# Optimization experiments

Measured on AMD Instinct MI355X. Metric: run time of the kernel, lower is better.

Reference implementation:

```python
import jax, jax.numpy as jnp
import numpy as np

V, D, K, NB, T = 50257, 128, 3, 8, 64
DIV_W = 2.0  # diversity_weight


def setup_inputs() -> dict:
    key = jax.random.key(0)
    k1, k2, k3 = jax.random.split(key, 3)
    tokens = jax.random.randint(k1, (T,), 0, V)
    E = jax.random.normal(k2, (V, D), jnp.float32)          # embedding table
    bubbles = 1.5 * jax.random.normal(k3, (K, NB, D), jnp.float32)  # init_spread_foam scale=1.5
    decay_base = jnp.asarray(0.8, jnp.float32)
    sensitivity = jnp.asarray(1.0, jnp.float32)
    return {"tokens": tokens, "E": E, "bubbles": bubbles,
            "decay_base": decay_base, "sensitivity": sensitivity}


def reference(tokens, E, bubbles, decay_base, sensitivity):
    d = E.shape[1]
    inv_sqrt_d = 1.0 / jnp.sqrt(jnp.asarray(d, jnp.float32))
    # normalized bubble states (pure-state directions), fixed over time
    psi = bubbles / (jnp.linalg.norm(bubbles, axis=-1, keepdims=True) + 1e-10)  # [K,NB,D]

    def step(memories, tok):
        # memories: [K, NB, D]
        x = E[tok]  # [D]
        mem_mean = memories.mean(axis=1)  # [K, D]
        mem_norm = jnp.linalg.norm(mem_mean, axis=-1) + 1e-10  # [K]
        x_norm = jnp.linalg.norm(x) + 1e-10
        cos = (mem_mean @ x) / (x_norm * mem_norm)  # [K]
        novelty = jnp.where(mem_norm > 1e-8, 1.0 - cos, 1.0)  # [K]
        decay = jax.nn.sigmoid(decay_base - jnp.abs(sensitivity) * novelty)  # [K]
        xm = x[None, :] + decay[:, None] * mem_mean  # [K, D]

        # foam forward (vectorized over K foams)
        scores = DIV_W * jnp.einsum('knd,kd->kn', bubbles, xm) * inv_sqrt_d  # [K,NB]
        w = jax.nn.softmax(scores, axis=-1)  # [K,NB]
        rho_k = jnp.einsum('kn,knd,kne->kde', w, psi, psi)  # [K,D,D] PSD, trace 1
        eq = w[..., None] * xm[:, None, :] + (1.0 - w)[..., None] * bubbles  # [K,NB,D]
        new_mem = decay[:, None, None] * memories + (1.0 - decay)[:, None, None] * eq

        rho = rho_k.mean(axis=0)  # [D,D] ensemble mixture
        eigs = jnp.clip(jnp.linalg.eigvalsh(rho), 1e-12)
        eigs = eigs / eigs.sum()
        logits = jnp.einsum('vd,de,ve->v', E, rho, E)  # born rule, [V]
        token_probs = jax.nn.softmax(logits)
        S_rho = -(eigs * jnp.clip(jnp.log(eigs), -100.0)).sum()
        H_tokens = -(token_probs * jnp.clip(jnp.log(token_probs), -100.0)).sum()
        F_tokens = H_tokens - S_rho
        logits_k = jnp.einsum('vd,kde,ve->kv', E, rho_k, E)  # [K,V]
        per_foam_probs = jax.nn.softmax(logits_k, axis=-1)
        return new_mem, (token_probs, rho, S_rho, H_tokens, F_tokens, per_foam_probs)

    mem0 = jnp.zeros((bubbles.shape[0], bubbles.shape[1], E.shape[1]), E.dtype)
    _, outs = jax.lax.scan(step, mem0, tokens)
    # outs: token_probs [T,V], rho [T,D,D], S_rho [T], H_tokens [T], F_tokens [T], per_foam_probs [T,K,V]
    return outs
```

## Files before the change

### kernel.cpp

```cpp
#include <hip/hip_runtime.h>
#include <math.h>

namespace {
constexpr int Vv  = 50257;
constexpr int Dc  = 128;
constexpr int Kc  = 3;
constexpr int NBc = 8;
constexpr int Jc  = 24;
constexpr int Tc  = 64;
constexpr int CHV = 1024;
constexpr int NCH = (Vv + CHV - 1) / CHV;
constexpr float INV_SQRT_D = 0.08838834764831845f;
constexpr float DIVW = 2.0f;

constexpr size_t WS_PSI  = 0;
constexpr size_t WS_G    = 4096;
constexpr size_t WS_BB   = 5120;
constexpr size_t WS_XN   = 6144;
constexpr size_t WS_BX   = 6400;
constexpr size_t WS_WALL = 8192;
constexpr size_t WS_PART = 12288;
constexpr size_t WS_LOGZ = 45056;
constexpr size_t WS_P2T  = 65536;

constexpr size_t OFF_TOK = 0;
constexpr size_t OFF_RHO = (size_t)Tc * Vv;
constexpr size_t OFF_S   = OFF_RHO + (size_t)Tc * Dc * Dc;
constexpr size_t OFF_H   = OFF_S + Tc;
constexpr size_t OFF_F   = OFF_H + Tc;
constexpr size_t OFF_PF  = OFF_F + Tc;
}

__device__ __forceinline__ float wsum64(float v) {
#pragma unroll
  for (int m = 1; m < 64; m <<= 1) v += __shfl_xor(v, m);
  return v;
}

__device__ __forceinline__ void comb(float& m1, float& s1, float m2, float s2) {
  float M = fmaxf(m1, m2);
  float e1 = (s1 > 0.f) ? expf(m1 - M) : 0.f;
  float e2 = (s2 > 0.f) ? expf(m2 - M) : 0.f;
  s1 = s1 * e1 + s2 * e2;
  m1 = M;
}
__device__ __forceinline__ void comb_sl(float& m1, float& s1, float& sl1,
                                        float m2, float s2, float sl2) {
  float M = fmaxf(m1, m2);
  float e1 = (s1 > 0.f) ? expf(m1 - M) : 0.f;
  float e2 = (s2 > 0.f) ? expf(m2 - M) : 0.f;
  s1 = s1 * e1 + s2 * e2;
  sl1 = sl1 * e1 + sl2 * e2;
  m1 = M;
}

__global__ void k_prep(const float* __restrict__ bub, float* __restrict__ ws) {
  __shared__ float braw[Jc * Dc];
  __shared__ float psi[Jc * Dc];
  __shared__ float nrm[Jc];
  int tid = threadIdx.x;
  for (int i = tid; i < Jc * Dc; i += 256) braw[i] = bub[i];
  __syncthreads();
  if (tid < Jc) {
    float s = 0.f;
    for (int d = 0; d < Dc; ++d) { float b = braw[tid * Dc + d]; s += b * b; }
    nrm[tid] = sqrtf(s) + 1e-10f;
  }
  __syncthreads();
  for (int i = tid; i < Jc * Dc; i += 256) {
    float v = braw[i] / nrm[i / Dc];
    psi[i] = v;
    ws[WS_PSI + i] = v;
  }
  __syncthreads();
  for (int i = tid; i < Jc * Jc; i += 256) {
    int r = i / Jc, c = i % Jc;
    float g = 0.f, b = 0.f;
    for (int d = 0; d < Dc; ++d) {
      g += psi[r * Dc + d] * psi[c * Dc + d];
      b += braw[r * Dc + d] * braw[c * Dc + d];
    }
    ws[WS_G + i] = g;
    ws[WS_BB + i] = b;
  }
}

__global__ void k_tok(const int* __restrict__ tok, const float* __restrict__ E,
                      const float* __restrict__ bub, float* __restrict__ ws) {
  int t = blockIdx.x, lane = threadIdx.x;
  int tk = tok[t];
  float eA = E[(size_t)tk * Dc + lane];
  float eB = E[(size_t)tk * Dc + 64 + lane];
  float xn = wsum64(eA * eA + eB * eB);
  if (lane == 0) ws[WS_XN + t] = xn;
  float p[Jc];
#pragma unroll
  for (int j = 0; j < Jc; ++j)
    p[j] = bub[j * Dc + lane] * eA + bub[j * Dc + 64 + lane] * eB;
#pragma unroll
  for (int j = 0; j < Jc; ++j) p[j] = wsum64(p[j]);
  if (lane == 0) {
#pragma unroll
    for (int j = 0; j < Jc; ++j) ws[WS_BX + (size_t)t * Jc + j] = p[j];
  }
}

__global__ void k_recur(const int* __restrict__ tok, const float* __restrict__ E,
                        const float* __restrict__ bub, const float* __restrict__ pdb,
                        const float* __restrict__ psn, float* __restrict__ ws) {
  __shared__ float sBX[Tc * Jc];
  __shared__ float sXN[Tc];
  int lane = threadIdx.x;
  for (int i = lane; i < Tc * Jc; i += 64) sBX[i] = ws[WS_BX + i];
  if (lane < Tc) sXN[lane] = ws[WS_XN + lane];
  float db = pdb[0];
  float sens = fabsf(psn[0]);
  int tokv = tok[lane];
  float bubA[Jc], bubB[Jc];
#pragma unroll
  for (int j = 0; j < Jc; ++j) {
    bubA[j] = bub[j * Dc + lane];
    bubB[j] = bub[j * Dc + 64 + lane];
  }
  int jme = (lane < Jc) ? lane : (Jc - 1);
  int kme = jme >> 3;
  float BBrow[Jc];
#pragma unroll
  for (int j = 0; j < Jc; ++j) BBrow[j] = ws[WS_BB + (size_t)jme * Jc + j];
  __syncthreads();
  float mmA[Kc] = {0.f, 0.f, 0.f}, mmB[Kc] = {0.f, 0.f, 0.f};
  float BMv[Kc] = {0.f, 0.f, 0.f};
  int tk0 = __shfl(tokv, 0);
  float xA = E[(size_t)tk0 * Dc + lane];
  float xB = E[(size_t)tk0 * Dc + 64 + lane];
  for (int t = 0; t < Tc; ++t) {
    float nxA = 0.f, nxB = 0.f;
    if (t + 1 < Tc) {
      int nk = __shfl(tokv, t + 1);
      nxA = E[(size_t)nk * Dc + lane];
      nxB = E[(size_t)nk * Dc + 64 + lane];
    }
    float dk[Kc], nk2[Kc];
#pragma unroll
    for (int k = 0; k < Kc; ++k) {
      dk[k]  = wsum64(mmA[k] * xA + mmB[k] * xB);
      nk2[k] = wsum64(mmA[k] * mmA[k] + mmB[k] * mmB[k]);
    }
    float xn = sqrtf(sXN[t]) + 1e-10f;
    float dec[Kc], xmA[Kc], xmB[Kc];
#pragma unroll
    for (int k = 0; k < Kc; ++k) {
      float mn = sqrtf(nk2[k]) + 1e-10f;
      float cosv = dk[k] / (xn * mn);
      float nov = (mn > 1e-8f) ? (1.f - cosv) : 1.f;
      dec[k] = 1.f / (1.f + expf(-(db - sens * nov)));
      xmA[k] = xA + dec[k] * mmA[k];
      xmB[k] = xB + dec[k] * mmB[k];
    }
    float bxj = sBX[t * Jc + jme];
    float decS = (kme == 0) ? dec[0] : ((kme == 1) ? dec[1] : dec[2]);
    float sc = (bxj + decS * BMv[kme]) * (DIVW * INV_SQRT_D);
    float mx = sc;
    mx = fmaxf(mx, __shfl_xor(mx, 1));
    mx = fmaxf(mx, __shfl_xor(mx, 2));
    mx = fmaxf(mx, __shfl_xor(mx, 4));
    float e = expf(sc - mx);
    float ss = e;
    ss += __shfl_xor(ss, 1);
    ss += __shfl_xor(ss, 2);
    ss += __shfl_xor(ss, 4);
    float w = e / ss;
    if (lane < Jc) ws[WS_WALL + (size_t)t * Jc + lane] = w;
    float wj[Jc];
#pragma unroll
    for (int j = 0; j < Jc; ++j) wj[j] = __shfl(w, j);
#pragma unroll
    for (int k = 0; k < Kc; ++k) {
      float accA = 0.f, accB = 0.f;
#pragma unroll
      for (int n = 0; n < NBc; ++n) {
        float om = 1.f - wj[k * NBc + n];
        accA += om * bubA[k * NBc + n];
        accB += om * bubB[k * NBc + n];
      }
      float od8 = (1.f - dec[k]) * 0.125f;
      mmA[k] = dec[k] * mmA[k] + od8 * (xmA[k] + accA);
      mmB[k] = dec[k] * mmB[k] + od8 * (xmB[k] + accB);
    }
#pragma unroll
    for (int k = 0; k < Kc; ++k) {
      float bxm = bxj + dec[k] * BMv[k];
      float s2 = 0.f;
#pragma unroll
      for (int n = 0; n < NBc; ++n) s2 += (1.f - wj[k * NBc + n]) * BBrow[k * NBc + n];
      BMv[k] = dec[k] * BMv[k] + (1.f - dec[k]) * 0.125f * (bxm + s2);
    }
    xA = nxA; xB = nxB;
  }
}

__global__ void k_proj(const float* __restrict__ E, float* __restrict__ ws) {
  __shared__ float4 psi4[Jc][Dc / 4];
  int tid = threadIdx.x;
  for (int i = tid; i < Jc * Dc / 4; i += 256)
    ((float4*)psi4)[i] = ((const float4*)(ws + WS_PSI))[i];
  __syncthreads();
  int v = blockIdx.x * 256 + tid;
  if (v >= Vv) return;
  float acc[Jc];
#pragma unroll
  for (int j = 0; j < Jc; ++j) acc[j] = 0.f;
  const float4* e4 = (const float4*)(E + (size_t)v * Dc);
  for (int d = 0; d < Dc / 4; ++d) {
    float4 e = e4[d];
#pragma unroll
    for (int j = 0; j < Jc; ++j) {
      float4 p = psi4[j][d];
      acc[j] += e.x * p.x + e.y * p.y + e.z * p.z + e.w * p.w;
    }
  }
#pragma unroll
  for (int j = 0; j < Jc; ++j) ws[WS_P2T + (size_t)j * Vv + v] = acc[j] * acc[j];
}

__global__ void k_rho(const float* __restrict__ ws, float* __restrict__ out) {
  int t = blockIdx.x;
  __shared__ float psis[Jc * Dc];
  __shared__ float wsh[Jc];
  int tid = threadIdx.x;
  for (int i = tid; i < Jc * Dc; i += 256) psis[i] = ws[WS_PSI + i];
  if (tid < Jc) wsh[tid] = ws[WS_WALL + (size_t)t * Jc + tid] * (1.f / 3.f);
  __syncthreads();
  int d = tid >> 1, eh = (tid & 1) * 64;
  float4 acc[16];
#pragma unroll
  for (int i = 0; i < 16; ++i) acc[i] = make_float4(0.f, 0.f, 0.f, 0.f);
  for (int j = 0; j < Jc; ++j) {
    float a = wsh[j] * psis[j * Dc + d];
    const float4* pr = (const float4*)&psis[j * Dc + eh];
#pragma unroll
    for (int i = 0; i < 16; ++i) {
      float4 p = pr[i];
      acc[i].x += a * p.x; acc[i].y += a * p.y; acc[i].z += a * p.z; acc[i].w += a * p.w;
    }
  }
  float* o = out + OFF_RHO + (size_t)t * Dc * Dc + (size_t)d * Dc + eh;
#pragma unroll
  for (int i = 0; i < 16; ++i) ((float4*)o)[i] = acc[i];
}

__global__ void k_eig(const float* __restrict__ ws, float* __restrict__ out) {
  int t = blockIdx.x;
  __shared__ float A[Jc * 25];
  int lane = threadIdx.x;
  for (int i = lane; i < Jc * Jc; i += 64) {
    int r = i / Jc, c = i % Jc;
    A[r * 25 + c] = ws[WS_G + i] *
                    sqrtf(ws[WS_WALL + (size_t)t * Jc + r] * ws[WS_WALL + (size_t)t * Jc + c]) *
                    (1.f / 3.f);
  }
  __syncthreads();
  for (int sweep = 0; sweep < 7; ++sweep) {
    for (int rr = 0; rr < 23; ++rr) {
      float cv = 1.f, sv = 0.f;
      if (lane < Jc) {
        int j = lane;
        int m = (j == 23) ? rr : ((j == rr) ? 23 : (2 * rr + 23 - j) % 23);
        int lo = min(j, m), hi = max(j, m);
        float ajj = A[j * 25 + j];
        float alh = A[lo * 25 + hi];
        float amm = __shfl(ajj, m);
        float app = (j == lo) ? ajj : amm;
        float aqq = (j == lo) ? amm : ajj;
        if (fabsf(alh) > 1e-20f) {
          float th = (aqq - app) / (2.f * alh);
          float tt = 1.f / (fabsf(th) + sqrtf(1.f + th * th));
          if (th < 0.f) tt = -tt;
          cv = 1.f / sqrtf(1.f + tt * tt);
          sv = tt * cv;
        }
      }
      __builtin_amdgcn_wave_barrier();
#pragma unroll
      for (int it = 0; it < 3; ++it) {
        int b = lane + 64 * it;
        int bb = (b < 144) ? b : 143;
        int pi = bb / 12, pj = bb % 12;
        int p0, q0, p1, q1;
        if (pi == 0) { p0 = rr; q0 = 23; }
        else { int a = (rr + pi) % 23, b2 = (rr + 23 - pi) % 23; p0 = min(a, b2); q0 = max(a, b2); }
        if (pj == 0) { p1 = rr; q1 = 23; }
        else { int a = (rr + pj) % 23, b2 = (rr + 23 - pj) % 23; p1 = min(a, b2); q1 = max(a, b2); }
        float ci = __shfl(cv, p0), si = __shfl(sv, p0);
        float cj = __shfl(cv, p1), sj = __shfl(sv, p1);
        if (b < 144) {
          float m00 = A[p0 * 25 + p1], m01 = A[p0 * 25 + q1];
          float m10 = A[q0 * 25 + p1], m11 = A[q0 * 25 + q1];
          float r00 = ci * m00 - si * m10, r01 = ci * m01 - si * m11;
          float r10 = si * m00 + ci * m10, r11 = si * m01 + ci * m11;
          float o00 = cj * r00 - sj * r01, o01 = sj * r00 + cj * r01;
          float o10 = cj * r10 - sj * r11, o11 = sj * r10 + cj * r11;
          A[p0 * 25 + p1] = o00; A[p0 * 25 + q1] = o01;
          A[q0 * 25 + p1] = o10; A[q0 * 25 + q1] = o11;
        }
      }
      __builtin_amdgcn_wave_barrier();
    }
  }
  float lam = 0.f;
  if (lane < Jc) lam = fmaxf(A[lane * 25 + lane], 1e-12f);
  float tot = lam;
#pragma unroll
  for (int off = 32; off; off >>= 1) tot += __shfl_down(tot, off);
  tot = __shfl(tot, 0);
  tot += (float)(Dc - Jc) * 1e-12f;
  float term = 0.f;
  if (lane < Jc) { float p = lam / tot; term = p * logf(p); }
#pragma unroll
  for (int off = 32; off; off >>= 1) term += __shfl_down(term, off);
  if (lane == 0) {
    float pe = 1e-12f / tot;
    out[OFF_S + t] = -(term + (float)(Dc - Jc) * pe * logf(pe));
  }
}

__global__ void k_logits(float* __restrict__ ws, float* __restrict__ out) {
  int ch = blockIdx.x, t = blockIdx.y, tid = threadIdx.x;
  __shared__ float wsh[Jc];
  __shared__ float rm[4][4], rs[4][4], rsl2[4];
  if (tid < Jc) wsh[tid] = ws[WS_WALL + (size_t)t * Jc + tid];
  __syncthreads();
  float m[4] = {-INFINITY, -INFINITY, -INFINITY, -INFINITY};
  float s[4] = {0.f, 0.f, 0.f, 0.f};
  float sl = 0.f;
  const float* p2 = ws + WS_P2T;
  for (int r = 0; r < 4; ++r) {
    int v = ch * CHV + r * 256 + tid;
    if (v >= Vv) break;
    float l0 = 0.f, l1 = 0.f, l2 = 0.f;
#pragma unroll
    for (int n = 0; n < NBc; ++n) {
      l0 += wsh[n]      * p2[(size_t)n * Vv + v];
      l1 += wsh[8 + n]  * p2[(size_t)(8 + n) * Vv + v];
      l2 += wsh[16 + n] * p2[(size_t)(16 + n) * Vv + v];
    }
    float l[4] = { l0, l1, l2, (l0 + l1 + l2) * (1.f / 3.f) };
    out[OFF_TOK + (size_t)t * Vv + v] = l[3];
    out[OFF_PF + ((size_t)t * Kc + 0) * Vv + v] = l0;
    out[OFF_PF + ((size_t)t * Kc + 1) * Vv + v] = l1;
    out[OFF_PF + ((size_t)t * Kc + 2) * Vv + v] = l2;
#pragma unroll
    for (int d = 0; d < 4; ++d) {
      float li = l[d];
      if (li > m[d]) {
        float e = expf(m[d] - li);
        s[d] = s[d] * e + 1.f;
        if (d == 3) sl = sl * e + li;
        m[d] = li;
      } else {
        float e = expf(li - m[d]);
        s[d] += e;
        if (d == 3) sl += e * li;
      }
    }
  }
#pragma unroll
  for (int off = 32; off; off >>= 1) {
#pragma unroll
    for (int d = 0; d < 3; ++d) {
      float om = __shfl_down(m[d], off);
      float os = __shfl_down(s[d], off);
      comb(m[d], s[d], om, os);
    }
    float om = __shfl_down(m[3], off);
    float os = __shfl_down(s[3], off);
    float osl = __shfl_down(sl, off);
    comb_sl(m[3], s[3], sl, om, os, osl);
  }
  int wv = tid >> 6, ln = tid & 63;
  if (ln == 0) {
#pragma unroll
    for (int d = 0; d < 4; ++d) { rm[wv][d] = m[d]; rs[wv][d] = s[d]; }
    rsl2[wv] = sl;
  }
  __syncthreads();
  if (tid == 0) {
    float* part = ws + WS_PART + ((size_t)t * NCH + ch) * 9;
    for (int d = 0; d < 3; ++d) {
      float M = rm[0][d], S = rs[0][d];
      for (int w2 = 1; w2 < 4; ++w2) comb(M, S, rm[w2][d], rs[w2][d]);
      part[d] = M; part[4 + d] = S;
    }
    float M = rm[0][3], S = rs[0][3], SL = rsl2[0];
    for (int w2 = 1; w2 < 4; ++w2) comb_sl(M, S, SL, rm[w2][3], rs[w2][3], rsl2[w2]);
    part[3] = M; part[7] = S; part[8] = SL;
  }
}

__global__ void k_reduce(float* __restrict__ ws, float* __restrict__ out) {
  int t = blockIdx.x, tid = threadIdx.x;
  if (tid < 4) {
    float M = -INFINITY, S = 0.f, SL = 0.f;
    for (int ch = 0; ch < NCH; ++ch) {
      const float* p = ws + WS_PART + ((size_t)t * NCH + ch) * 9;
      if (tid == 3) comb_sl(M, S, SL, p[3], p[7], p[8]);
      else          comb(M, S, p[tid], p[4 + tid]);
    }
    float lz = M + logf(S);
    ws[WS_LOGZ + (size_t)t * 4 + tid] = lz;
    if (tid == 3) {
      float H = lz - SL / S;
      float Srho = out[OFF_S + t];
      out[OFF_H + t] = H;
      out[OFF_F + t] = H - Srho;
    }
  }
}

__global__ void k_norm(const float* __restrict__ ws, float* __restrict__ out, int foam) {
  int row = blockIdx.y, ch = blockIdx.x, tid = threadIdx.x;
  size_t base; int lzi;
  if (foam) { int t = row / Kc, k = row % Kc; base = OFF_PF + (size_t)row * Vv; lzi = t * 4 + k; }
  else { base = OFF_TOK + (size_t)row * Vv; lzi = row * 4 + 3; }
  float lz = ws[WS_LOGZ + lzi];
  for (int r = 0; r < 4; ++r) {
    int v = ch * CHV + r * 256 + tid;
    if (v < Vv) out[base + v] = expf(out[base + v] - lz);
  }
}

extern "C" void kernel_launch(void* const* d_in, const int* in_sizes, int n_in,
                              void* d_out, int out_size, void* d_ws, size_t ws_size,
                              hipStream_t stream) {
  const int*   tokens = (const int*)d_in[0];
  const float* E      = (const float*)d_in[1];
  const float* bub    = (const float*)d_in[2];
  const float* pdb    = (const float*)d_in[3];
  const float* psn    = (const float*)d_in[4];
  float* out = (float*)d_out;
  float* ws  = (float*)d_ws;

  k_prep<<<1, 256, 0, stream>>>(bub, ws);
  k_proj<<<(Vv + 255) / 256, 256, 0, stream>>>(E, ws);
  k_tok<<<Tc, 64, 0, stream>>>(tokens, E, bub, ws);
  k_recur<<<1, 64, 0, stream>>>(tokens, E, bub, pdb, psn, ws);
  k_rho<<<Tc, 256, 0, stream>>>(ws, out);
  k_eig<<<Tc, 64, 0, stream>>>(ws, out);
  k_logits<<<dim3(NCH, Tc), 256, 0, stream>>>(ws, out);
  k_reduce<<<Tc, 64, 0, stream>>>(ws, out);
  k_norm<<<dim3(NCH, Tc), 256, 0, stream>>>(ws, out, 0);
  k_norm<<<dim3(NCH, Tc * Kc), 256, 0, stream>>>(ws, out, 1);
}
```

Measured before the change: 499.9 us.

## Keep Jacobi eigen matrix in registers with lane-per-row rotations

Rewrites the per-timestep Jacobi eigenvalue kernel so each lane holds one row of the 24x24 Gram matrix in registers, instead of keeping the matrix in shared memory. Column rotations use compile-time pair tables and readlane, and row rotations use cross-lane shuffles, with the whole rr loop fully unrolled. The aim is to remove LDS traffic, wave barriers and index arithmetic. In exchange it raises register pressure, grows code size, and adds a mux-tree select for dynamic indexing. The k_eig kernel is a small part of total time next to the logits kernels.

```diff
diff --git a/kernel.cpp b/kernel.cpp
--- a/kernel.cpp
+++ b/kernel.cpp
@@ -29,12 +29,51 @@
 constexpr size_t OFF_H   = OFF_S + Tc;
 constexpr size_t OFF_F   = OFF_H + Tc;
 constexpr size_t OFF_PF  = OFF_F + Tc;
+
+struct PairTab { int lo[23][12]; int hi[23][12]; };
+constexpr PairTab make_pairs() {
+  PairTab P{};
+  for (int rr = 0; rr < 23; ++rr) {
+    int idx = 0;
+    P.lo[rr][idx] = rr; P.hi[rr][idx] = 23; ++idx;
+    bool used[24] = {};
+    used[rr] = true; used[23] = true;
+    for (int j = 0; j < 23; ++j) {
+      if (used[j]) continue;
+      int mj = (2 * rr + 23 - j) % 23;
+      int lo = j < mj ? j : mj, hi = j < mj ? mj : j;
+      used[lo] = true; used[hi] = true;
+      P.lo[rr][idx] = lo; P.hi[rr][idx] = hi; ++idx;
+    }
+  }
+  return P;
+}
+constexpr PairTab PT = make_pairs();
 }
 
 __device__ __forceinline__ float wsum64(float v) {
 #pragma unroll
   for (int m = 1; m < 64; m <<= 1) v += __shfl_xor(v, m);
   return v;
+}
+
+__device__ __forceinline__ float sel24(const float (&m)[Jc], int idx) {
+  bool b0 = (idx & 1) != 0, b1 = (idx & 2) != 0, b2 = (idx & 4) != 0;
+  float t[12];
+#pragma unroll
+  for (int i = 0; i < 12; ++i) t[i] = b0 ? m[2 * i + 1] : m[2 * i];
+  float u[6];
+#pragma unroll
+  for (int i = 0; i < 6; ++i) u[i] = b1 ? t[2 * i + 1] : t[2 * i];
+  float v[3];
+#pragma unroll
+  for (int i = 0; i < 3; ++i) v[i] = b2 ? u[2 * i + 1] : u[2 * i];
+  int g = idx >> 3;
+  return (g == 0) ? v[0] : ((g == 1) ? v[1] : v[2]);
+}
+
+__device__ __forceinline__ float rdlane(float v, int lane) {
+  return __int_as_float(__builtin_amdgcn_readlane(__float_as_int(v), lane));
 }
 
 __device__ __forceinline__ void comb(float& m1, float& s1, float m2, float s2) {
@@ -251,64 +290,58 @@
 
 __global__ void k_eig(const float* __restrict__ ws, float* __restrict__ out) {
   int t = blockIdx.x;
-  __shared__ float A[Jc * 25];
   int lane = threadIdx.x;
-  for (int i = lane; i < Jc * Jc; i += 64) {
-    int r = i / Jc, c = i % Jc;
-    A[r * 25 + c] = ws[WS_G + i] *
-                    sqrtf(ws[WS_WALL + (size_t)t * Jc + r] * ws[WS_WALL + (size_t)t * Jc + c]) *
-                    (1.f / 3.f);
-  }
-  __syncthreads();
+  int jme = (lane < Jc) ? lane : (Jc - 1);
+  float w_me = ws[WS_WALL + (size_t)t * Jc + jme];
+  float m[Jc];
+#pragma unroll
+  for (int r = 0; r < Jc; ++r) {
+    float wr = ws[WS_WALL + (size_t)t * Jc + r];
+    m[r] = ws[WS_G + (size_t)jme * Jc + r] * sqrtf(wr * w_me) * (1.f / 3.f);
+  }
+#pragma unroll 1
   for (int sweep = 0; sweep < 7; ++sweep) {
+#pragma unroll
     for (int rr = 0; rr < 23; ++rr) {
+      int x = 2 * rr + 23 - jme;
+      if (x >= 23) x -= 23;
+      if (x >= 23) x -= 23;
+      int pr = (jme == 23) ? rr : ((jme == rr) ? 23 : x);
+      float d_own = sel24(m, jme);
+      float a_own = sel24(m, pr);
+      float dq = __shfl(d_own, pr);
+      float aq = __shfl(a_own, pr);
+      bool isLo = jme < pr;
+      float apq = isLo ? a_own : aq;
+      float app = isLo ? d_own : dq;
+      float aqq = isLo ? dq : d_own;
       float cv = 1.f, sv = 0.f;
-      if (lane < Jc) {
-        int j = lane;
-        int m = (j == 23) ? rr : ((j == rr) ? 23 : (2 * rr + 23 - j) % 23);
-        int lo = min(j, m), hi = max(j, m);
-        float ajj = A[j * 25 + j];
-        float alh = A[lo * 25 + hi];
-        float amm = __shfl(ajj, m);
-        float app = (j == lo) ? ajj : amm;
-        float aqq = (j == lo) ? amm : ajj;
-        if (fabsf(alh) > 1e-20f) {
-          float th = (aqq - app) / (2.f * alh);
-          float tt = 1.f / (fabsf(th) + sqrtf(1.f + th * th));
-          if (th < 0.f) tt = -tt;
-          cv = 1.f / sqrtf(1.f + tt * tt);
-          sv = tt * cv;
-        }
+      if (fabsf(apq) > 1e-20f) {
+        float th = (aqq - app) / (2.f * apq);
+        float tt = 1.f / (fabsf(th) + sqrtf(1.f + th * th));
+        if (th < 0.f) tt = -tt;
+        cv = 1.f / sqrtf(1.f + tt * tt);
+        sv = tt * cv;
       }
-      __builtin_amdgcn_wave_barrier();
-#pragma unroll
-      for (int it = 0; it < 3; ++it) {
-        int b = lane + 64 * it;
-        int bb = (b < 144) ? b : 143;
-        int pi = bb / 12, pj = bb % 12;
-        int p0, q0, p1, q1;
-        if (pi == 0) { p0 = rr; q0 = 23; }
-        else { int a = (rr + pi) % 23, b2 = (rr + 23 - pi) % 23; p0 = min(a, b2); q0 = max(a, b2); }
-        if (pj == 0) { p1 = rr; q1 = 23; }
-        else { int a = (rr + pj) % 23, b2 = (rr + 23 - pj) % 23; p1 = min(a, b2); q1 = max(a, b2); }
-        float ci = __shfl(cv, p0), si = __shfl(sv, p0);
-        float cj = __shfl(cv, p1), sj = __shfl(sv, p1);
-        if (b < 144) {
-          float m00 = A[p0 * 25 + p1], m01 = A[p0 * 25 + q1];
-          float m10 = A[q0 * 25 + p1], m11 = A[q0 * 25 + q1];
-          float r00 = ci * m00 - si * m10, r01 = ci * m01 - si * m11;
-          float r10 = si * m00 + ci * m10, r11 = si * m01 + ci * m11;
-          float o00 = cj * r00 - sj * r01, o01 = sj * r00 + cj * r01;
-          float o10 = cj * r10 - sj * r11, o11 = sj * r10 + cj * r11;
-          A[p0 * 25 + p1] = o00; A[p0 * 25 + q1] = o01;
-          A[q0 * 25 + p1] = o10; A[q0 * 25 + q1] = o11;
-        }
+#pragma unroll
+      for (int i = 0; i < 12; ++i) {
+        const int p = PT.lo[rr][i], q = PT.hi[rr][i];
+        float ci = rdlane(cv, p);
+        float si = rdlane(sv, p);
+        float tp = m[p];
+        m[p] = ci * tp - si * m[q];
+        m[q] = si * tp + ci * m[q];
       }
-      __builtin_amdgcn_wave_barrier();
-    }
-  }
-  float lam = 0.f;
-  if (lane < Jc) lam = fmaxf(A[lane * 25 + lane], 1e-12f);
+      float seff = isLo ? -sv : sv;
+#pragma unroll
+      for (int r = 0; r < Jc; ++r) {
+        float y = __shfl(m[r], pr);
+        m[r] = cv * m[r] + seff * y;
+      }
+    }
+  }
+  float lam = sel24(m, jme);
+  lam = (lane < Jc) ? fmaxf(lam, 1e-12f) : 0.f;
   float tot = lam;
 #pragma unroll
   for (int off = 32; off; off >>= 1) tot += __shfl_down(tot, off);
```

Measured after the change: 675.2 us. 35.1% more time.
